# Optimization experiments

Hardware: AMD Instinct MI355X
Metric: run time of the kernel (lower is better)

Reference implementation:

```python
import jax, jax.numpy as jnp
import numpy as np

B = 131072
D_IN = 385          # 384-d embedding + 1 correctness feature
D_H = 192           # both trunk layers resolve to max(.,192)=192 per source
Q = 1000            # number of questions
C = 16              # classes per head (uniform padding of per-question heads)


def setup_inputs() -> dict:
    key = jax.random.key(0)
    ks = jax.random.split(key, 9)
    x = jax.random.normal(ks[0], (B, D_IN), dtype=jnp.float32)
    question_ids = jax.random.randint(ks[1], (B,), 0, Q, dtype=jnp.int32)
    is_correct = jax.random.randint(ks[2], (B,), 0, 2, dtype=jnp.int32)
    W1 = jax.random.normal(ks[3], (D_IN, D_H), dtype=jnp.float32) * 0.05
    b1 = jnp.zeros((D_H,), dtype=jnp.float32)
    W2 = jax.random.normal(ks[4], (D_H, D_H), dtype=jnp.float32) * 0.05
    b2 = jnp.zeros((D_H,), dtype=jnp.float32)
    # Head bank: slots [0,Q) = false heads, [Q,2Q) = true heads.
    W_heads = jax.random.normal(ks[5], (2 * Q, C, D_H), dtype=jnp.float32) * 0.05
    b_heads = jax.random.normal(ks[6], (2 * Q, C), dtype=jnp.float32) * 0.05
    return {"x": x, "question_ids": question_ids, "is_correct": is_correct,
            "W1": W1, "b1": b1, "W2": W2, "b2": b2,
            "W_heads": W_heads, "b_heads": b_heads}


def reference(x, question_ids, is_correct, W1, b1, W2, b2, W_heads, b_heads):
    # Shared trunk (eval mode: dropout = identity)
    h = jax.nn.relu(x @ W1 + b1)            # [B, 192]
    feat = jax.nn.relu(h @ W2 + b2)         # [B, 192]
    # Hard routing: pick true or false head for this question.
    Qn = W_heads.shape[0] // 2
    idx = question_ids + is_correct * Qn    # [B]
    Wq = W_heads[idx]                       # [B, C, 192] gather (memory-bound)
    bq = b_heads[idx]                       # [B, C]
    logits = jnp.einsum('bcd,bd->bc', Wq, feat) + bq  # per-sample routed linear
    return logits
```

## Files before the change

### kernel.cpp

```cpp
#include <hip/hip_runtime.h>
#include <stdint.h>
#include <stddef.h>


typedef short s8v __attribute__((ext_vector_type(8)));
typedef float f4v __attribute__((ext_vector_type(4)));
typedef float f4a __attribute__((ext_vector_type(4), aligned(4)));

namespace {
constexpr int kDin = 385;
constexpr int kDh  = 192;
constexpr int kQ   = 1000;
constexpr int kC   = 16;
constexpr int BM   = 64;
constexpr int NT   = 256;
constexpr int NK1  = 13;
constexpr int NK2  = 6;
constexpr int CHUNK = 12 * 64 * 8;
constexpr int H2   = 200;

constexpr size_t WS_W1   = 0;
constexpr size_t WS_W2   = 163840;
constexpr size_t WS_HIST = 245760;
constexpr size_t WS_CUR  = 253952;
constexpr size_t WS_PERM = 262144;
}

__device__ __forceinline__ unsigned short f2bf(float f) {
  unsigned int u = __float_as_uint(f);
  u = u + 0x7fffu + ((u >> 16) & 1u);
  return (unsigned short)(u >> 16);
}

__device__ __forceinline__ void swz_one(const float* W, int K, int i,
                                        unsigned short* out) {
  int k = i / kDh;
  int c = i - k * kDh;
  float v = (k < K) ? W[(size_t)k * kDh + c] : 0.f;
  int oi = (k >> 5) * CHUNK + (((c >> 4) * 64 + ((k >> 3) & 3) * 16 + (c & 15)) << 3)
         + (k & 7);
  out[oi] = f2bf(v);
}

__global__ void combo_prep(const int* __restrict__ qid, const int* __restrict__ isc,
                           int B, int nbH,
                           const float* __restrict__ W1, const float* __restrict__ W2,
                           int* __restrict__ hist,
                           unsigned short* __restrict__ W1sw,
                           unsigned short* __restrict__ W2sw) {
  int bid = blockIdx.x;
  if (bid < nbH) {
    int i = bid * 256 + threadIdx.x;
    if (i < B) atomicAdd(&hist[qid[i] + isc[i] * kQ], 1);
  } else if (bid < nbH + 312) {
    swz_one(W1, kDin, (bid - nbH) * 256 + threadIdx.x, W1sw);
  } else {
    swz_one(W2, kDh, (bid - nbH - 312) * 256 + threadIdx.x, W2sw);
  }
}

__global__ void scan_k(const int* __restrict__ hist, int* __restrict__ cursor) {
  __shared__ int s[2048];
  int t = threadIdx.x;
  s[t] = hist[t]; s[t + 1024] = hist[t + 1024];
  __syncthreads();
  for (int d = 1; d < 2048; d <<= 1) {
    int a0 = (t >= d) ? s[t - d] : 0;
    int a1 = (t + 1024 >= d) ? s[t + 1024 - d] : 0;
    __syncthreads();
    s[t] += a0; s[t + 1024] += a1;
    __syncthreads();
  }
  cursor[t] = s[t] - hist[t];
  cursor[t + 1024] = s[t + 1024] - hist[t + 1024];
}

__global__ void scatter_k(const int* __restrict__ qid, const int* __restrict__ isc,
                          int B, int* __restrict__ cursor, int* __restrict__ perm) {
  int i = blockIdx.x * blockDim.x + threadIdx.x;
  if (i < B) {
    int h = qid[i] + isc[i] * kQ;
    int pos = atomicAdd(&cursor[h], 1);
    perm[pos] = i;
  }
}

__global__ __launch_bounds__(NT, 4)
void fused_qmlp5(const float* __restrict__ x,
                 const int*   __restrict__ qid,
                 const int*   __restrict__ isc,
                 const float* __restrict__ b1,
                 const float* __restrict__ b2,
                 const float* __restrict__ Wh,
                 const float* __restrict__ bh,
                 const unsigned short* __restrict__ W1sw,
                 const unsigned short* __restrict__ W2sw,
                 const int*   __restrict__ perm,
                 float* __restrict__ out) {
  __shared__ __align__(16) unsigned short hS[BM * H2];
  __shared__ __align__(16) unsigned short bS[CHUNK];
  __shared__ int permS[BM];
  __shared__ int idxS[BM];

  const int tid  = threadIdx.x;
  const int lane = tid & 63, wid = tid >> 6;
  const int m = lane & 15, quad = lane >> 4;
  const int rh = wid & 1, ch = wid >> 1;
  const int row0 = blockIdx.x * BM;

  if (tid < BM) {
    int p = perm[row0 + tid];
    permS[tid] = p;
    idxS[tid] = qid[p] + isc[p] * kQ;
  }
  __syncthreads();

  const size_t xr0 = (size_t)permS[rh * 32 + m] * kDin;
  const size_t xr1 = (size_t)permS[rh * 32 + m + 16] * kDin;

  f4v acc0[6], acc1[6];
  #pragma unroll
  for (int t = 0; t < 6; ++t) {
    acc0[t] = (f4v){0.f, 0.f, 0.f, 0.f};
    acc1[t] = (f4v){0.f, 0.f, 0.f, 0.f};
  }

  for (int kk = 0; kk < NK1; ++kk) {
    const s8v* src = (const s8v*)(W1sw + (size_t)kk * CHUNK);
    s8v w0 = src[tid], w1 = src[tid + NT], w2 = src[tid + 2 * NT];

    s8v a0, a1;
    if (kk < NK1 - 1) {
      const float* p0 = x + xr0 + kk * 32 + quad * 8;
      const float* p1 = x + xr1 + kk * 32 + quad * 8;
      f4a v00 = *(const f4a*)p0, v01 = *(const f4a*)(p0 + 4);
      f4a v10 = *(const f4a*)p1, v11 = *(const f4a*)(p1 + 4);
      #pragma unroll
      for (int j = 0; j < 4; ++j) {
        a0[j]     = (short)f2bf(v00[j]);
        a0[j + 4] = (short)f2bf(v01[j]);
        a1[j]     = (short)f2bf(v10[j]);
        a1[j + 4] = (short)f2bf(v11[j]);
      }
    } else {
      float v0 = (quad == 0) ? x[xr0 + 384] : 0.f;
      float v1 = (quad == 0) ? x[xr1 + 384] : 0.f;
      a0 = (s8v){0,0,0,0,0,0,0,0};
      a1 = (s8v){0,0,0,0,0,0,0,0};
      a0[0] = (short)f2bf(v0);
      a1[0] = (short)f2bf(v1);
    }

    ((s8v*)bS)[tid] = w0;
    ((s8v*)bS)[tid + NT] = w1;
    ((s8v*)bS)[tid + 2 * NT] = w2;
    __syncthreads();

    #pragma unroll
    for (int t = 0; t < 6; ++t) {
      s8v b = *(const s8v*)&bS[((ch * 6 + t) * 64 + lane) * 8];
      acc0[t] = __builtin_amdgcn_mfma_f32_16x16x32_bf16(a0, b, acc0[t], 0, 0, 0);
      acc1[t] = __builtin_amdgcn_mfma_f32_16x16x32_bf16(a1, b, acc1[t], 0, 0, 0);
    }
    __syncthreads();
  }

  #pragma unroll
  for (int t = 0; t < 6; ++t) {
    int c = ch * 96 + t * 16 + m;
    float bb = b1[c];
    #pragma unroll
    for (int r4 = 0; r4 < 4; ++r4) {
      int r = rh * 32 + quad * 4 + r4;
      float v0 = acc0[t][r4] + bb; v0 = v0 > 0.f ? v0 : 0.f;
      hS[r * H2 + c] = f2bf(v0);
      float v1 = acc1[t][r4] + bb; v1 = v1 > 0.f ? v1 : 0.f;
      hS[(r + 16) * H2 + c] = f2bf(v1);
      acc0[t][r4] = 0.f;
      acc1[t][r4] = 0.f;
    }
  }

  const int ar0 = (rh * 32 + m) * H2;
  for (int kk = 0; kk < NK2; ++kk) {
    const s8v* src = (const s8v*)(W2sw + (size_t)kk * CHUNK);
    s8v w0 = src[tid], w1 = src[tid + NT], w2 = src[tid + 2 * NT];
    ((s8v*)bS)[tid] = w0;
    ((s8v*)bS)[tid + NT] = w1;
    ((s8v*)bS)[tid + 2 * NT] = w2;
    __syncthreads();

    s8v a0 = *(const s8v*)&hS[ar0 + kk * 32 + quad * 8];
    s8v a1 = *(const s8v*)&hS[ar0 + 16 * H2 + kk * 32 + quad * 8];
    #pragma unroll
    for (int t = 0; t < 6; ++t) {
      s8v b = *(const s8v*)&bS[((ch * 6 + t) * 64 + lane) * 8];
      acc0[t] = __builtin_amdgcn_mfma_f32_16x16x32_bf16(a0, b, acc0[t], 0, 0, 0);
      acc1[t] = __builtin_amdgcn_mfma_f32_16x16x32_bf16(a1, b, acc1[t], 0, 0, 0);
    }
    __syncthreads();
  }

  #pragma unroll
  for (int t = 0; t < 6; ++t) {
    int c = ch * 96 + t * 16 + m;
    float bb = b2[c];
    #pragma unroll
    for (int r4 = 0; r4 < 4; ++r4) {
      int r = rh * 32 + quad * 4 + r4;
      float v0 = acc0[t][r4] + bb;
      hS[r * H2 + c] = f2bf(v0 > 0.f ? v0 : 0.f);
      float v1 = acc1[t][r4] + bb;
      hS[(r + 16) * H2 + c] = f2bf(v1 > 0.f ? v1 : 0.f);
    }
  }
  __syncthreads();

  {
    const int w16 = wid * 16;
    const int hm = idxS[w16 + m];
    unsigned rem = 0xFFFFu;
    while (rem) {
      int r0 = (int)__builtin_ctz(rem);
      int h = idxS[w16 + r0];
      unsigned long long bal = __ballot(hm == h);
      unsigned mask16 = (unsigned)(bal & 0xFFFFu);
      rem &= ~mask16;
      bool valid = (hm == h);

      const float* wq = Wh + ((size_t)h * kC + m) * kDh + quad * 8;
      f4v acc = (f4v){0.f, 0.f, 0.f, 0.f};
      #pragma unroll
      for (int kk = 0; kk < 6; ++kk) {
        float4 wlo = *(const float4*)(wq + kk * 32);
        float4 whi = *(const float4*)(wq + kk * 32 + 4);
        s8v bfr;
        bfr[0] = (short)f2bf(wlo.x); bfr[1] = (short)f2bf(wlo.y);
        bfr[2] = (short)f2bf(wlo.z); bfr[3] = (short)f2bf(wlo.w);
        bfr[4] = (short)f2bf(whi.x); bfr[5] = (short)f2bf(whi.y);
        bfr[6] = (short)f2bf(whi.z); bfr[7] = (short)f2bf(whi.w);
        s8v afr = *(const s8v*)&hS[(w16 + m) * H2 + kk * 32 + quad * 8];
        if (!valid) afr = (s8v){0,0,0,0,0,0,0,0};
        acc = __builtin_amdgcn_mfma_f32_16x16x32_bf16(afr, bfr, acc, 0, 0, 0);
      }
      float bhv = bh[(size_t)h * kC + m];
      #pragma unroll
      for (int reg = 0; reg < 4; ++reg) {
        int r = quad * 4 + reg;
        if ((mask16 >> r) & 1u)
          out[(size_t)permS[w16 + r] * kC + m] = acc[reg] + bhv;
      }
    }
  }
}

extern "C" void kernel_launch(void* const* d_in, const int* in_sizes, int n_in,
                              void* d_out, int out_size, void* d_ws, size_t ws_size,
                              hipStream_t stream) {
  const float* x  = (const float*)d_in[0];
  const int*   qd = (const int*)  d_in[1];
  const int*   ic = (const int*)  d_in[2];
  const float* W1 = (const float*)d_in[3];
  const float* b1 = (const float*)d_in[4];
  const float* W2 = (const float*)d_in[5];
  const float* b2 = (const float*)d_in[6];
  const float* Wh = (const float*)d_in[7];
  const float* bh = (const float*)d_in[8];
  float* out = (float*)d_out;

  char* ws = (char*)d_ws;
  unsigned short* W1sw = (unsigned short*)(ws + WS_W1);
  unsigned short* W2sw = (unsigned short*)(ws + WS_W2);
  int* hist   = (int*)(ws + WS_HIST);
  int* cursor = (int*)(ws + WS_CUR);
  int* perm   = (int*)(ws + WS_PERM);

  int B = in_sizes[1];
  int nbH = (B + 255) / 256;

  hipMemsetAsync(hist, 0, 2048 * sizeof(int), stream);
  combo_prep<<<nbH + 312 + 144, 256, 0, stream>>>(qd, ic, B, nbH, W1, W2,
                                                  hist, W1sw, W2sw);
  scan_k<<<1, 1024, 0, stream>>>(hist, cursor);
  scatter_k<<<(B + 255) / 256, 256, 0, stream>>>(qd, ic, B, cursor, perm);

  fused_qmlp5<<<B / BM, NT, 0, stream>>>(x, qd, ic, b1, b2, Wh, bh,
                                         W1sw, W2sw, perm, out);
}
```

Before: 396.2 us.

## Double-buffer weight chunks via direct global-to-LDS loads and fuse scan into scatter

```diff
diff --git a/kernel.cpp b/kernel.cpp
--- a/kernel.cpp
+++ b/kernel.cpp
@@ -1,4 +1,5 @@
 #include <hip/hip_runtime.h>
+#include <hip/hip_bf16.h>
 #include <stdint.h>
 #include <stddef.h>
 
@@ -6,6 +7,9 @@
 typedef short s8v __attribute__((ext_vector_type(8)));
 typedef float f4v __attribute__((ext_vector_type(4)));
 typedef float f4a __attribute__((ext_vector_type(4), aligned(4)));
+
+typedef const void __attribute__((address_space(1))) *gas1_t;
+typedef void __attribute__((address_space(3))) *las3_t;
 
 namespace {
 constexpr int kDin = 385;
@@ -31,6 +35,14 @@
   u = u + 0x7fffu + ((u >> 16) & 1u);
   return (unsigned short)(u >> 16);
 }
+
+__device__ __forceinline__ unsigned int pk2(float lo, float hi) {
+  union { __hip_bfloat162 h2; unsigned int u; } cv;
+  cv.h2 = __float22bfloat162_rn(make_float2(lo, hi));
+  return cv.u;
+}
+
+union s8u { s8v s; unsigned int u[4]; };
 
 __device__ __forceinline__ void swz_one(const float* W, int K, int i,
                                         unsigned short* out) {
@@ -59,34 +71,55 @@
   }
 }
 
-__global__ void scan_k(const int* __restrict__ hist, int* __restrict__ cursor) {
-  __shared__ int s[2048];
+__global__ __launch_bounds__(256)
+void scatter2(const int* __restrict__ qid, const int* __restrict__ isc, int B,
+              const int* __restrict__ hist, int* __restrict__ rank_ctr,
+              int* __restrict__ perm) {
+  __shared__ int sh[2048];
+  __shared__ int ssum[256];
   int t = threadIdx.x;
-  s[t] = hist[t]; s[t + 1024] = hist[t + 1024];
-  __syncthreads();
-  for (int d = 1; d < 2048; d <<= 1) {
-    int a0 = (t >= d) ? s[t - d] : 0;
-    int a1 = (t + 1024 >= d) ? s[t + 1024 - d] : 0;
+  int4 a = ((const int4*)hist)[t * 2];
+  int4 b = ((const int4*)hist)[t * 2 + 1];
+  int s1 = a.x + a.y, s2 = s1 + a.z, s3 = s2 + a.w;
+  int s4 = s3 + b.x, s5 = s4 + b.y, s6 = s5 + b.z, s7 = s6 + b.w;
+  ssum[t] = s7;
+  __syncthreads();
+  #pragma unroll
+  for (int d = 1; d < 256; d <<= 1) {
+    int xv = (t >= d) ? ssum[t - d] : 0;
     __syncthreads();
-    s[t] += a0; s[t + 1024] += a1;
+    ssum[t] += xv;
     __syncthreads();
   }
-  cursor[t] = s[t] - hist[t];
-  cursor[t + 1024] = s[t + 1024] - hist[t + 1024];
-}
-
-__global__ void scatter_k(const int* __restrict__ qid, const int* __restrict__ isc,
-                          int B, int* __restrict__ cursor, int* __restrict__ perm) {
-  int i = blockIdx.x * blockDim.x + threadIdx.x;
+  int base = ssum[t] - s7;
+  sh[t * 8 + 0] = base;
+  sh[t * 8 + 1] = base + a.x;
+  sh[t * 8 + 2] = base + s1;
+  sh[t * 8 + 3] = base + s2;
+  sh[t * 8 + 4] = base + s3;
+  sh[t * 8 + 5] = base + s4;
+  sh[t * 8 + 6] = base + s5;
+  sh[t * 8 + 7] = base + s6;
+  __syncthreads();
+  int i = blockIdx.x * 256 + t;
   if (i < B) {
     int h = qid[i] + isc[i] * kQ;
-    int pos = atomicAdd(&cursor[h], 1);
+    int pos = sh[h] + atomicAdd(&rank_ctr[h], 1);
     perm[pos] = i;
   }
 }
 
-__global__ __launch_bounds__(NT, 4)
-void fused_qmlp5(const float* __restrict__ x,
+__device__ __forceinline__ void stage_chunk(const unsigned short* gsrc,
+                                            unsigned short* lbase, int tid) {
+  const char* g = (const char*)gsrc + (size_t)tid * 16;
+  char* l = (char*)lbase + ((tid >> 6) << 10);
+  __builtin_amdgcn_global_load_lds((gas1_t)g,          (las3_t)l,          16, 0, 0);
+  __builtin_amdgcn_global_load_lds((gas1_t)(g + 4096), (las3_t)(l + 4096), 16, 0, 0);
+  __builtin_amdgcn_global_load_lds((gas1_t)(g + 8192), (las3_t)(l + 8192), 16, 0, 0);
+}
+
+__global__ __launch_bounds__(NT, 3)
+void fused_qmlp6(const float* __restrict__ x,
                  const int*   __restrict__ qid,
                  const int*   __restrict__ isc,
                  const float* __restrict__ b1,
@@ -98,7 +131,7 @@
                  const int*   __restrict__ perm,
                  float* __restrict__ out) {
   __shared__ __align__(16) unsigned short hS[BM * H2];
-  __shared__ __align__(16) unsigned short bS[CHUNK];
+  __shared__ __align__(16) unsigned short bS[2 * CHUNK];
   __shared__ int permS[BM];
   __shared__ int idxS[BM];
 
@@ -113,10 +146,11 @@
     permS[tid] = p;
     idxS[tid] = qid[p] + isc[p] * kQ;
   }
-  __syncthreads();
-
-  const size_t xr0 = (size_t)permS[rh * 32 + m] * kDin;
-  const size_t xr1 = (size_t)permS[rh * 32 + m + 16] * kDin;
+  stage_chunk(W1sw, bS, tid);
+  __syncthreads();
+
+  const float* px0 = x + (size_t)permS[rh * 32 + m] * kDin;
+  const float* px1 = x + (size_t)permS[rh * 32 + m + 16] * kDin;
 
   f4v acc0[6], acc1[6];
   #pragma unroll
@@ -125,44 +159,58 @@
     acc1[t] = (f4v){0.f, 0.f, 0.f, 0.f};
   }
 
+  f4a c0, c1, c2, c3;
+  {
+    const float* q0 = px0 + quad * 8;
+    const float* q1 = px1 + quad * 8;
+    c0 = *(const f4a*)q0; c1 = *(const f4a*)(q0 + 4);
+    c2 = *(const f4a*)q1; c3 = *(const f4a*)(q1 + 4);
+  }
+  float tl0 = 0.f, tl1 = 0.f;
+
+  #pragma unroll
   for (int kk = 0; kk < NK1; ++kk) {
-    const s8v* src = (const s8v*)(W1sw + (size_t)kk * CHUNK);
-    s8v w0 = src[tid], w1 = src[tid + NT], w2 = src[tid + 2 * NT];
+    const int nj = kk + 1;
+    const unsigned short* np = (nj < NK1)
+        ? W1sw + (size_t)nj * CHUNK
+        : W2sw;
+    stage_chunk(np, bS + (nj & 1) * CHUNK, tid);
+
+    f4a n0, n1, n2, n3;
+    if (kk < NK1 - 2) {
+      const float* q0 = px0 + nj * 32 + quad * 8;
+      const float* q1 = px1 + nj * 32 + quad * 8;
+      n0 = *(const f4a*)q0; n1 = *(const f4a*)(q0 + 4);
+      n2 = *(const f4a*)q1; n3 = *(const f4a*)(q1 + 4);
+    } else if (kk == NK1 - 2) {
+      tl0 = (quad == 0) ? px0[384] : 0.f;
+      tl1 = (quad == 0) ? px1[384] : 0.f;
+    }
 
     s8v a0, a1;
     if (kk < NK1 - 1) {
-      const float* p0 = x + xr0 + kk * 32 + quad * 8;
-      const float* p1 = x + xr1 + kk * 32 + quad * 8;
-      f4a v00 = *(const f4a*)p0, v01 = *(const f4a*)(p0 + 4);
-      f4a v10 = *(const f4a*)p1, v11 = *(const f4a*)(p1 + 4);
-      #pragma unroll
-      for (int j = 0; j < 4; ++j) {
-        a0[j]     = (short)f2bf(v00[j]);
-        a0[j + 4] = (short)f2bf(v01[j]);
-        a1[j]     = (short)f2bf(v10[j]);
-        a1[j + 4] = (short)f2bf(v11[j]);
-      }
+      s8u ua, ub;
+      ua.u[0] = pk2(c0[0], c0[1]); ua.u[1] = pk2(c0[2], c0[3]);
+      ua.u[2] = pk2(c1[0], c1[1]); ua.u[3] = pk2(c1[2], c1[3]);
+      ub.u[0] = pk2(c2[0], c2[1]); ub.u[1] = pk2(c2[2], c2[3]);
+      ub.u[2] = pk2(c3[0], c3[1]); ub.u[3] = pk2(c3[2], c3[3]);
+      a0 = ua.s; a1 = ub.s;
     } else {
-      float v0 = (quad == 0) ? x[xr0 + 384] : 0.f;
-      float v1 = (quad == 0) ? x[xr1 + 384] : 0.f;
       a0 = (s8v){0,0,0,0,0,0,0,0};
       a1 = (s8v){0,0,0,0,0,0,0,0};
-      a0[0] = (short)f2bf(v0);
-      a1[0] = (short)f2bf(v1);
-    }
-
-    ((s8v*)bS)[tid] = w0;
-    ((s8v*)bS)[tid + NT] = w1;
-    ((s8v*)bS)[tid + 2 * NT] = w2;
-    __syncthreads();
-
+      a0[0] = (short)f2bf(tl0);
+      a1[0] = (short)f2bf(tl1);
+    }
+
+    const unsigned short* bBuf = bS + (kk & 1) * CHUNK;
     #pragma unroll
     for (int t = 0; t < 6; ++t) {
-      s8v b = *(const s8v*)&bS[((ch * 6 + t) * 64 + lane) * 8];
+      s8v b = *(const s8v*)&bBuf[((ch * 6 + t) * 64 + lane) * 8];
       acc0[t] = __builtin_amdgcn_mfma_f32_16x16x32_bf16(a0, b, acc0[t], 0, 0, 0);
       acc1[t] = __builtin_amdgcn_mfma_f32_16x16x32_bf16(a1, b, acc1[t], 0, 0, 0);
     }
     __syncthreads();
+    if (kk < NK1 - 2) { c0 = n0; c1 = n1; c2 = n2; c3 = n3; }
   }
 
   #pragma unroll
@@ -180,21 +228,21 @@
       acc1[t][r4] = 0.f;
     }
   }
+  __syncthreads();
 
   const int ar0 = (rh * 32 + m) * H2;
-  for (int kk = 0; kk < NK2; ++kk) {
-    const s8v* src = (const s8v*)(W2sw + (size_t)kk * CHUNK);
-    s8v w0 = src[tid], w1 = src[tid + NT], w2 = src[tid + 2 * NT];
-    ((s8v*)bS)[tid] = w0;
-    ((s8v*)bS)[tid + NT] = w1;
-    ((s8v*)bS)[tid + 2 * NT] = w2;
-    __syncthreads();
-
-    s8v a0 = *(const s8v*)&hS[ar0 + kk * 32 + quad * 8];
-    s8v a1 = *(const s8v*)&hS[ar0 + 16 * H2 + kk * 32 + quad * 8];
+  #pragma unroll
+  for (int k2 = 0; k2 < NK2; ++k2) {
+    if (k2 < NK2 - 1)
+      stage_chunk(W2sw + (size_t)(k2 + 1) * CHUNK,
+                  bS + ((14 + k2) & 1) * CHUNK, tid);
+
+    s8v a0 = *(const s8v*)&hS[ar0 + k2 * 32 + quad * 8];
+    s8v a1 = *(const s8v*)&hS[ar0 + 16 * H2 + k2 * 32 + quad * 8];
+    const unsigned short* bBuf = bS + ((13 + k2) & 1) * CHUNK;
     #pragma unroll
     for (int t = 0; t < 6; ++t) {
-      s8v b = *(const s8v*)&bS[((ch * 6 + t) * 64 + lane) * 8];
+      s8v b = *(const s8v*)&bBuf[((ch * 6 + t) * 64 + lane) * 8];
       acc0[t] = __builtin_amdgcn_mfma_f32_16x16x32_bf16(a0, b, acc0[t], 0, 0, 0);
       acc1[t] = __builtin_amdgcn_mfma_f32_16x16x32_bf16(a1, b, acc1[t], 0, 0, 0);
     }
@@ -234,11 +282,12 @@
       for (int kk = 0; kk < 6; ++kk) {
         float4 wlo = *(const float4*)(wq + kk * 32);
         float4 whi = *(const float4*)(wq + kk * 32 + 4);
-        s8v bfr;
-        bfr[0] = (short)f2bf(wlo.x); bfr[1] = (short)f2bf(wlo.y);
-        bfr[2] = (short)f2bf(wlo.z); bfr[3] = (short)f2bf(wlo.w);
-        bfr[4] = (short)f2bf(whi.x); bfr[5] = (short)f2bf(whi.y);
-        bfr[6] = (short)f2bf(whi.z); bfr[7] = (short)f2bf(whi.w);
+        s8u ub;
+        ub.u[0] = pk2(wlo.x, wlo.y);
+        ub.u[1] = pk2(wlo.z, wlo.w);
+        ub.u[2] = pk2(whi.x, whi.y);
+        ub.u[3] = pk2(whi.z, whi.w);
+        s8v bfr = ub.s;
         s8v afr = *(const s8v*)&hS[(w16 + m) * H2 + kk * 32 + quad * 8];
         if (!valid) afr = (s8v){0,0,0,0,0,0,0,0};
         acc = __builtin_amdgcn_mfma_f32_16x16x32_bf16(afr, bfr, acc, 0, 0, 0);
@@ -271,19 +320,18 @@
   char* ws = (char*)d_ws;
   unsigned short* W1sw = (unsigned short*)(ws + WS_W1);
   unsigned short* W2sw = (unsigned short*)(ws + WS_W2);
-  int* hist   = (int*)(ws + WS_HIST);
-  int* cursor = (int*)(ws + WS_CUR);
-  int* perm   = (int*)(ws + WS_PERM);
+  int* hist = (int*)(ws + WS_HIST);
+  int* rank = (int*)(ws + WS_CUR);
+  int* perm = (int*)(ws + WS_PERM);
 
   int B = in_sizes[1];
   int nbH = (B + 255) / 256;
 
-  hipMemsetAsync(hist, 0, 2048 * sizeof(int), stream);
+  hipMemsetAsync(hist, 0, 4096 * sizeof(int), stream);
   combo_prep<<<nbH + 312 + 144, 256, 0, stream>>>(qd, ic, B, nbH, W1, W2,
                                                   hist, W1sw, W2sw);
-  scan_k<<<1, 1024, 0, stream>>>(hist, cursor);
-  scatter_k<<<(B + 255) / 256, 256, 0, stream>>>(qd, ic, B, cursor, perm);
-
-  fused_qmlp5<<<B / BM, NT, 0, stream>>>(x, qd, ic, b1, b2, Wh, bh,
+  scatter2<<<(B + 255) / 256, 256, 0, stream>>>(qd, ic, B, hist, rank, perm);
+
+  fused_qmlp6<<<B / BM, NT, 0, stream>>>(x, qd, ic, b1, b2, Wh, bh,
                                          W1sw, W2sw, perm, out);
 }
```

Measured after the change: 413.1 us. 4.3% more time.
